# Optimization experiments

Measured on AMD Instinct MI355X. Metric: run time of the kernel, lower is better.

The kernel has to match this reference:

```python
import jax, jax.numpy as jnp
import numpy as np

DIM = 768
H = 12
HD = 64  # head_dim = dim // num_heads
SCALE = HD ** (-0.5)
EPS = 1e-6


def setup_inputs() -> dict:
    key = jax.random.key(0)
    k1, k2, k3, k4, k5 = jax.random.split(key, 5)
    B, N = 8, 1024
    x = jax.random.normal(k1, (B, N, DIM), dtype=jnp.float32)
    policy = jax.random.uniform(k2, (B, N, 1), dtype=jnp.float32)
    # nn.Linear weights: [out_features, in_features]; qkv_bias=False, proj has bias
    qkv_w = jax.random.normal(k3, (3 * H * HD, DIM), dtype=jnp.float32) * (DIM ** -0.5)
    proj_w = jax.random.normal(k4, (DIM, H * HD), dtype=jnp.float32) * ((H * HD) ** -0.5)
    proj_b = jax.random.normal(k5, (DIM,), dtype=jnp.float32) * 0.01
    return {"x": x, "policy": policy, "qkv_w": qkv_w, "proj_w": proj_w, "proj_b": proj_b}


def _softmax_with_policy(attn, policy):
    # attn: [B,H,N,N], policy: [B,N,1]
    B, Hh, N, _ = attn.shape
    attn_policy = policy.reshape(B, 1, 1, N)
    eye = jnp.eye(N, dtype=attn_policy.dtype).reshape(1, 1, N, N)
    attn_policy = attn_policy + (1.0 - attn_policy) * eye
    max_att = jnp.max(attn, axis=-1, keepdims=True)
    a = jnp.exp((attn - max_att).astype(jnp.float32)) * attn_policy.astype(jnp.float32)
    a = (a + EPS / N) / (jnp.sum(a, axis=-1, keepdims=True) + EPS)
    return a.astype(max_att.dtype)


def reference(x, policy, qkv_w, proj_w, proj_b):
    B, N, C = x.shape
    qkv = (x @ qkv_w.T).reshape(B, N, 3, H, HD)
    qkv = jnp.transpose(qkv, (2, 0, 3, 1, 4))  # [3,B,H,N,HD]
    q, k, v = qkv[0], qkv[1], qkv[2]
    attn = jnp.einsum('bhnd,bhmd->bhnm', q * SCALE, k)  # [B,H,N,N]
    attn = _softmax_with_policy(attn, policy)
    out = jnp.einsum('bhnm,bhmd->bhnd', attn, v)  # [B,H,N,HD]
    out = jnp.transpose(out, (0, 2, 1, 3)).reshape(B, N, H * HD)
    return out @ proj_w.T + proj_b
```

## Files before the change

### kernel.cpp

```cpp
#include <hip/hip_runtime.h>

typedef __bf16 bf16x8 __attribute__((ext_vector_type(8)));
typedef float floatx4 __attribute__((ext_vector_type(4)));

#define EPSF 1e-6f

__device__ inline unsigned short f2bf(float f) {
  union { float f; unsigned u; } x; x.f = f;
  unsigned r = x.u + 0x7FFFu + ((x.u >> 16) & 1u);
  return (unsigned short)(r >> 16);
}
__device__ inline float bf2f(unsigned short u) {
  union { unsigned u; float f; } x; x.u = ((unsigned)u) << 16;
  return x.f;
}
__device__ inline unsigned pk2bf(float lo, float hi) {
  union { float f; unsigned u; } a, b; a.f = lo; b.f = hi;
  unsigned ua = a.u + 0x8000u, ub = b.u + 0x8000u;
  return (ub & 0xFFFF0000u) | (ua >> 16);
}
__device__ inline float fexp2(float x) { return __builtin_amdgcn_exp2f(x); }

__device__ inline floatx4 mfma16(bf16x8 a, bf16x8 b, floatx4 c) {
  return __builtin_amdgcn_mfma_f32_16x16x32_bf16(a, b, c, 0, 0, 0);
}

__device__ inline void gll16(const unsigned short* g, unsigned short* l) {
  __builtin_amdgcn_global_load_lds((__attribute__((address_space(1))) void*)g,
                                   (__attribute__((address_space(3))) void*)l, 16, 0, 0);
}

__device__ __host__ inline int sigma_inv(int p) {
  const int qq = p >> 3, jj = p & 7;
  return (jj < 4) ? (qq * 4 + jj) : (16 + qq * 4 + jj - 4);
}

__global__ __launch_bounds__(256) void prep_kernel(const float* __restrict__ x,
                                                   const float* __restrict__ qkv_w,
                                                   const float* __restrict__ proj_w,
                                                   const float* __restrict__ policy,
                                                   unsigned short* __restrict__ xb,
                                                   unsigned short* __restrict__ wqkv,
                                                   unsigned short* __restrict__ wproj,
                                                   unsigned short* __restrict__ pbf) {
  const int bid = blockIdx.x, tid = threadIdx.x;
  if (bid < 3072) {
    const int i = bid * 2048 + tid * 8;
    float4 v0 = *(const float4*)(x + i);
    float4 v1 = *(const float4*)(x + i + 4);
    __align__(16) unsigned short o[8] = {f2bf(v0.x), f2bf(v0.y), f2bf(v0.z), f2bf(v0.w),
                                         f2bf(v1.x), f2bf(v1.y), f2bf(v1.z), f2bf(v1.w)};
    *(float4*)(xb + i) = *(float4*)o;
  } else if (bid < 3936) {
    const int i = (bid - 3072) * 2048 + tid * 8;
    const float s = (i < 589824) ? 0.18033688011112042f : 1.0f;
    float4 v0 = *(const float4*)(qkv_w + i);
    float4 v1 = *(const float4*)(qkv_w + i + 4);
    __align__(16) unsigned short o[8] = {
        f2bf(v0.x * s), f2bf(v0.y * s), f2bf(v0.z * s), f2bf(v0.w * s),
        f2bf(v1.x * s), f2bf(v1.y * s), f2bf(v1.z * s), f2bf(v1.w * s)};
    *(float4*)(wqkv + i) = *(float4*)o;
  } else if (bid < 4224) {
    const int i0 = (bid - 3936) * 2048 + tid * 8;
    const int base = (i0 / 768) * 768 + ((i0 % 768) & ~63);
    __align__(16) unsigned short o[8];
#pragma unroll
    for (int t = 0; t < 8; t++) {
      const int cp = (i0 + t) & 63;
      const int c = 16 * (cp & 3) + (cp >> 2);
      o[t] = f2bf(proj_w[base + c]);
    }
    *(float4*)(wproj + i0) = *(float4*)o;
  } else {
    const int idx = (bid - 4224) * 256 + tid;
    const int b = idx >> 10, g = idx & 1023;
    const int c = ((g >> 5) << 5) + sigma_inv(g & 31);
    pbf[idx] = f2bf(policy[b * 1024 + c]);
  }
}

template <int EP, int BN, int W>
__global__ __launch_bounds__(256, W) void gemm_bt(const unsigned short* __restrict__ A,
                                                  const unsigned short* __restrict__ Bt,
                                                  void* __restrict__ Cout,
                                                  const float* __restrict__ bias,
                                                  int M, int N, int K) {
  constexpr int J = BN / 32;
  __shared__ __align__(16) unsigned short sA[128 * 64];
  __shared__ __align__(16) unsigned short sB[BN * 64];
  const int bid = blockIdx.x;
  const int yb = (bid & 7) * 8 + ((bid >> 3) & 7);
  const int xb_ = bid >> 6;
  const int m0 = yb * 128, n0 = xb_ * BN;
  const int tid = threadIdx.x;
  const int lane = tid & 63, wave = tid >> 6;
  const int qd = lane >> 4, l15 = lane & 15;
  const int wr = (wave >> 1) * 64, wc = (wave & 1) * (BN / 2);
  const int srow = tid >> 3;
  const int scb = (tid & 7) ^ (srow & 7);
  const unsigned short* Ag = A + (long)(m0 + srow) * K + scb * 8;
  const unsigned short* Bg = Bt + (long)(n0 + srow) * K + scb * 8;
  const int x7 = l15 & 7;
  floatx4 acc[4][J] = {};
  for (int k0 = 0; k0 < K; k0 += 64) {
    __syncthreads();
#pragma unroll
    for (int p = 0; p < 4; p++) gll16(Ag + (long)(p * 32) * K + k0, sA + p * 2048 + wave * 512);
#pragma unroll
    for (int p = 0; p < J; p++) gll16(Bg + (long)(p * 32) * K + k0, sB + p * 2048 + wave * 512);
    __syncthreads();
#pragma unroll
    for (int s = 0; s < 2; s++) {
      const int cw = ((s * 4 + qd) ^ x7) * 8;
      bf16x8 af[4], bf[J];
#pragma unroll
      for (int i = 0; i < 4; i++) af[i] = *(const bf16x8*)&sA[(wr + i * 16 + l15) * 64 + cw];
#pragma unroll
      for (int j = 0; j < J; j++) bf[j] = *(const bf16x8*)&sB[(wc + j * 16 + l15) * 64 + cw];
#pragma unroll
      for (int i = 0; i < 4; i++)
#pragma unroll
        for (int j = 0; j < J; j++) acc[i][j] = mfma16(af[i], bf[j], acc[i][j]);
    }
  }
  if constexpr (EP == 0) {
#pragma unroll
    for (int i = 0; i < 4; i++)
#pragma unroll
      for (int r = 0; r < 4; r++) {
        const int row = m0 + wr + i * 16 + qd * 4 + r;
        __align__(8) unsigned short pk[4];
#pragma unroll
        for (int j = 0; j < 4; j++) pk[j] = f2bf(acc[i][j][r]);
        *(uint2*)((unsigned short*)Cout + (long)row * N + n0 + wc + 4 * l15) = *(uint2*)pk;
      }
  } else {
#pragma unroll
    for (int i = 0; i < 4; i++)
#pragma unroll
      for (int j = 0; j < J; j++) {
        const int col = n0 + wc + j * 16 + l15;
#pragma unroll
        for (int r = 0; r < 4; r++) {
          const int row = m0 + wr + i * 16 + qd * 4 + r;
          ((float*)Cout)[(long)row * N + col] = acc[i][j][r] + bias[col];
        }
      }
  }
}

__global__ __launch_bounds__(256) void transpose_v(const unsigned short* __restrict__ qkv,
                                                   const float* __restrict__ policy,
                                                   unsigned short* __restrict__ vTp) {
  __shared__ unsigned short tile[64][72];
  __shared__ float sPol[64];
  const int bh = blockIdx.y;
  const int b = bh / 12, h = bh % 12;
  const int n0 = blockIdx.x * 64;
  const int t = threadIdx.x;
  if (t < 64) sPol[t] = policy[b * 1024 + n0 + t];
  {
    const int nr = t >> 2, dc = (t & 3) * 16;
    const unsigned short* src = qkv + (long)(b * 1024 + n0 + nr) * 2304 + 2 * 768 + h * 64 + dc;
    float4 v0 = *(const float4*)src;
    float4 v1 = *(const float4*)(src + 8);
    *(float4*)&tile[nr][dc] = v0;
    *(float4*)&tile[nr][dc + 8] = v1;
  }
  __syncthreads();
  {
    const int d = t >> 2, nc = (t & 3) * 16;
    __align__(16) unsigned short o[16];
#pragma unroll
    for (int jj = 0; jj < 16; jj++) {
      const int cc = nc + jj;
      const int cl = (cc & 32) + sigma_inv(cc & 31);
      o[jj] = f2bf(bf2f(tile[cl][d]) * sPol[cl]);
    }
    unsigned short* dst = vTp + (long)(bh * 64 + d) * 1024 + n0 + nc;
    *(float4*)dst = *(float4*)&o[0];
    *(float4*)(dst + 8) = *(float4*)&o[8];
  }
}

__global__ __launch_bounds__(256, 3) void attn_kernel(const unsigned short* __restrict__ qkv,
                                                      const unsigned short* __restrict__ vTp,
                                                      const unsigned short* __restrict__ pbf,
                                                      const float* __restrict__ policy,
                                                      unsigned short* __restrict__ aout) {
  __shared__ __align__(16) unsigned short sK[2][2048];
  __shared__ __align__(16) unsigned short sV[2][2048];
  __shared__ __align__(16) unsigned short sPv[1024];
  __shared__ float sD[4][32];
  const int bid = blockIdx.x;
  const int bh = bid % 96, qt = bid / 96;
  const int b = bh / 12, h = bh % 12;
  const int tid = threadIdx.x;
  const int wave = tid >> 6, lane = tid & 63;
  const int qd = lane >> 4, l15 = lane & 15;
  const int q0 = qt * 128 + wave * 32;
  const unsigned short* qb = qkv + (long)(b * 1024 + q0 + l15) * 2304 + h * 64 + qd * 8;
  bf16x8 qf00 = *(const bf16x8*)qb;
  bf16x8 qf01 = *(const bf16x8*)(qb + 32);
  bf16x8 qf10 = *(const bf16x8*)(qb + (long)16 * 2304);
  bf16x8 qf11 = *(const bf16x8*)(qb + (long)16 * 2304 + 32);
  if (tid < 128) *(float4*)(sPv + tid * 8) = *(const float4*)(pbf + b * 1024 + tid * 8);
  const int krow = wave * 8 + (lane >> 3);
  const int kcb = (lane & 7) ^ (lane >> 3);
  const unsigned short* kgl = qkv + (long)(b * 1024 + krow) * 2304 + 768 + h * 64 + kcb * 8;
  const int vrow = tid >> 2;
  const int vcb = (tid & 3) ^ ((vrow ^ (vrow >> 2)) & 3);
  const unsigned short* vgl = vTp + (long)(bh * 64 + vrow) * 1024 + vcb * 8;
  const int x7 = l15 & 7;
  const int vsw = (qd ^ ((l15 ^ (l15 >> 2)) & 3)) * 8;
  floatx4 O0[4] = {}, O1[4] = {};
  floatx4 Dl0 = {}, Dl1 = {};
  gll16(kgl, &sK[0][wave * 512]);
  gll16(vgl, &sV[0][wave * 512]);
  __builtin_amdgcn_s_waitcnt(0);
  __syncthreads();
  for (int it = 0; it < 32; ++it) {
    const int buf = it & 1;
    if (it < 31) {
      gll16(kgl + (long)(32 * (it + 1)) * 2304, &sK[buf ^ 1][wave * 512]);
      gll16(vgl + 32 * (it + 1), &sV[buf ^ 1][wave * 512]);
    }
    const int c0 = it * 32;
    bf16x8 k00 = *(const bf16x8*)&sK[buf][(0 * 16 + l15) * 64 + ((0 + qd) ^ x7) * 8];
    bf16x8 k01 = *(const bf16x8*)&sK[buf][(0 * 16 + l15) * 64 + ((4 + qd) ^ x7) * 8];
    bf16x8 k10 = *(const bf16x8*)&sK[buf][(1 * 16 + l15) * 64 + ((0 + qd) ^ x7) * 8];
    bf16x8 k11 = *(const bf16x8*)&sK[buf][(1 * 16 + l15) * 64 + ((4 + qd) ^ x7) * 8];
    bf16x8 pv = *(const bf16x8*)&sPv[c0 + qd * 8];
    floatx4 z = {0.f, 0.f, 0.f, 0.f};
    floatx4 tA0 = mfma16(k01, qf01, mfma16(k00, qf00, z));
    floatx4 tB0 = mfma16(k11, qf01, mfma16(k10, qf00, z));
    floatx4 tA1 = mfma16(k01, qf11, mfma16(k00, qf10, z));
    floatx4 tB1 = mfma16(k11, qf11, mfma16(k10, qf10, z));
    uint4 pu0, pu1;
    pu0.x = pk2bf(fexp2(tA0[0]), fexp2(tA0[1]));
    pu0.y = pk2bf(fexp2(tA0[2]), fexp2(tA0[3]));
    pu0.z = pk2bf(fexp2(tB0[0]), fexp2(tB0[1]));
    pu0.w = pk2bf(fexp2(tB0[2]), fexp2(tB0[3]));
    pu1.x = pk2bf(fexp2(tA1[0]), fexp2(tA1[1]));
    pu1.y = pk2bf(fexp2(tA1[2]), fexp2(tA1[3]));
    pu1.z = pk2bf(fexp2(tB1[0]), fexp2(tB1[1]));
    pu1.w = pk2bf(fexp2(tB1[2]), fexp2(tB1[3]));
    bf16x8 pf0 = *(bf16x8*)&pu0;
    bf16x8 pf1 = *(bf16x8*)&pu1;
    bf16x8 vf0 = *(const bf16x8*)&sV[buf][(0 * 16 + l15) * 32 + vsw];
    bf16x8 vf1 = *(const bf16x8*)&sV[buf][(1 * 16 + l15) * 32 + vsw];
    bf16x8 vf2 = *(const bf16x8*)&sV[buf][(2 * 16 + l15) * 32 + vsw];
    bf16x8 vf3 = *(const bf16x8*)&sV[buf][(3 * 16 + l15) * 32 + vsw];
    Dl0 = mfma16(pf0, pv, Dl0);
    Dl1 = mfma16(pf1, pv, Dl1);
    O0[0] = mfma16(pf0, vf0, O0[0]); O1[0] = mfma16(pf1, vf0, O1[0]);
    O0[1] = mfma16(pf0, vf1, O0[1]); O1[1] = mfma16(pf1, vf1, O1[1]);
    O0[2] = mfma16(pf0, vf2, O0[2]); O1[2] = mfma16(pf1, vf2, O1[2]);
    O0[3] = mfma16(pf0, vf3, O0[3]); O1[3] = mfma16(pf1, vf3, O1[3]);
    __builtin_amdgcn_s_waitcnt(0);
    __syncthreads();
  }
  {
    const unsigned short* kd = qkv + (long)(b * 1024 + q0 + l15) * 2304 + 768 + h * 64 + qd * 8;
    bf16x8 kd00 = *(const bf16x8*)kd;
    bf16x8 kd01 = *(const bf16x8*)(kd + 32);
    bf16x8 kd10 = *(const bf16x8*)(kd + (long)16 * 2304);
    bf16x8 kd11 = *(const bf16x8*)(kd + (long)16 * 2304 + 32);
    float part0 = 0.f, part1 = 0.f;
#pragma unroll
    for (int jj = 0; jj < 8; jj++) {
      part0 += (float)qf00[jj] * (float)kd00[jj] + (float)qf01[jj] * (float)kd01[jj];
      part1 += (float)qf10[jj] * (float)kd10[jj] + (float)qf11[jj] * (float)kd11[jj];
    }
    part0 += __shfl_xor(part0, 16); part0 += __shfl_xor(part0, 32);
    part1 += __shfl_xor(part1, 16); part1 += __shfl_xor(part1, 32);
    const float p0 = policy[b * 1024 + q0 + l15];
    const float p1 = policy[b * 1024 + q0 + 16 + l15];
    if (qd == 0) {
      sD[wave][l15] = fexp2(part0) * (1.0f - p0);
      sD[wave][16 + l15] = fexp2(part1) * (1.0f - p1);
    }
    __builtin_amdgcn_s_waitcnt(0);
    const unsigned short* vdiag = qkv + (long)(b * 1024 + q0) * 2304 + 1536 + h * 64 + l15;
#pragma unroll
    for (int r = 0; r < 4; r++) {
      const int row = qd * 4 + r;
      const float c0v = sD[wave][row], c1v = sD[wave][16 + row];
#pragma unroll
      for (int j = 0; j < 4; j++) {
        O0[j][r] += c0v * bf2f(vdiag[(long)row * 2304 + j * 16]);
        O1[j][r] += c1v * bf2f(vdiag[(long)(16 + row) * 2304 + j * 16]);
      }
      Dl0[r] += c0v;
      Dl1[r] += c1v;
    }
  }
  const long ob = (long)(b * 1024 + q0 + qd * 4) * 768 + h * 64 + l15;
#pragma unroll
  for (int r = 0; r < 4; r++) {
    const float li0 = 1.0f / (Dl0[r] + EPSF);
    const float li1 = 1.0f / (Dl1[r] + EPSF);
#pragma unroll
    for (int j = 0; j < 4; j++) {
      aout[ob + (long)r * 768 + j * 16] = f2bf(O0[j][r] * li0);
      aout[ob + (long)(16 * 768) + r * 768 + j * 16] = f2bf(O1[j][r] * li1);
    }
  }
}

extern "C" void kernel_launch(void* const* d_in, const int* in_sizes, int n_in,
                              void* d_out, int out_size, void* d_ws, size_t ws_size,
                              hipStream_t stream) {
  const float* x      = (const float*)d_in[0];
  const float* policy = (const float*)d_in[1];
  const float* qkv_w  = (const float*)d_in[2];
  const float* proj_w = (const float*)d_in[3];
  const float* proj_b = (const float*)d_in[4];
  float* out = (float*)d_out;

  char* ws = (char*)d_ws;
  unsigned short* xb    = (unsigned short*)(ws + 0);
  unsigned short* wqkv  = (unsigned short*)(ws + 12582912);
  unsigned short* wproj = (unsigned short*)(ws + 16121856);
  unsigned short* qkvb  = (unsigned short*)(ws + 17301504);
  unsigned short* vTp   = (unsigned short*)(ws + 55050240);
  unsigned short* aoutb = (unsigned short*)(ws + 67633152);
  unsigned short* pbf   = (unsigned short*)(ws + 80216064);

  prep_kernel<<<4256, 256, 0, stream>>>(x, qkv_w, proj_w, policy, xb, wqkv, wproj, pbf);
  gemm_bt<0, 128, 4><<<dim3(18 * 64), 256, 0, stream>>>(xb, wqkv, qkvb, nullptr, 8192, 2304, 768);
  transpose_v<<<dim3(16, 96), 256, 0, stream>>>(qkvb, policy, vTp);
  attn_kernel<<<dim3(768), 256, 0, stream>>>(qkvb, vTp, pbf, policy, aoutb);
  gemm_bt<1, 64, 3><<<dim3(12 * 64), 256, 0, stream>>>(aoutb, wproj, out, proj_b, 8192, 768, 768);
}
```

Baseline: 175.6 us.

## Software-pipeline QK^T one tile ahead with triple-buffered V in attention loop

Restructures the attention main loop so the QK^T MFMAs for the next key tile are issued in the same iteration as the exp/PV work of the current tile. Global prefetch runs two tiles ahead, K stays double-buffered and V moves to a triple buffer so the in-flight loads do not overwrite tiles still being read. The aim is to overlap the exp2 VALU work with matrix-core work and hide load latency. In exchange it uses more LDS and more registers, which could reduce occupancy at launch bounds of 3 blocks.

```diff
diff --git a/kernel.cpp b/kernel.cpp
--- a/kernel.cpp
+++ b/kernel.cpp
@@ -189,7 +189,7 @@
                                                       const float* __restrict__ policy,
                                                       unsigned short* __restrict__ aout) {
   __shared__ __align__(16) unsigned short sK[2][2048];
-  __shared__ __align__(16) unsigned short sV[2][2048];
+  __shared__ __align__(16) unsigned short sV[3][2048];
   __shared__ __align__(16) unsigned short sPv[1024];
   __shared__ float sD[4][32];
   const int bid = blockIdx.x;
@@ -215,27 +215,30 @@
   const int vsw = (qd ^ ((l15 ^ (l15 >> 2)) & 3)) * 8;
   floatx4 O0[4] = {}, O1[4] = {};
   floatx4 Dl0 = {}, Dl1 = {};
+  const floatx4 z = {0.f, 0.f, 0.f, 0.f};
   gll16(kgl, &sK[0][wave * 512]);
   gll16(vgl, &sV[0][wave * 512]);
+  gll16(kgl + (long)32 * 2304, &sK[1][wave * 512]);
+  gll16(vgl + 32, &sV[1][wave * 512]);
   __builtin_amdgcn_s_waitcnt(0);
   __syncthreads();
+  floatx4 tA0, tB0, tA1, tB1;
+  {
+    bf16x8 k00 = *(const bf16x8*)&sK[0][(0 * 16 + l15) * 64 + ((0 + qd) ^ x7) * 8];
+    bf16x8 k01 = *(const bf16x8*)&sK[0][(0 * 16 + l15) * 64 + ((4 + qd) ^ x7) * 8];
+    bf16x8 k10 = *(const bf16x8*)&sK[0][(1 * 16 + l15) * 64 + ((0 + qd) ^ x7) * 8];
+    bf16x8 k11 = *(const bf16x8*)&sK[0][(1 * 16 + l15) * 64 + ((4 + qd) ^ x7) * 8];
+    tA0 = mfma16(k01, qf01, mfma16(k00, qf00, z));
+    tB0 = mfma16(k11, qf01, mfma16(k10, qf00, z));
+    tA1 = mfma16(k01, qf11, mfma16(k00, qf10, z));
+    tB1 = mfma16(k11, qf11, mfma16(k10, qf10, z));
+  }
   for (int it = 0; it < 32; ++it) {
-    const int buf = it & 1;
-    if (it < 31) {
-      gll16(kgl + (long)(32 * (it + 1)) * 2304, &sK[buf ^ 1][wave * 512]);
-      gll16(vgl + 32 * (it + 1), &sV[buf ^ 1][wave * 512]);
-    }
-    const int c0 = it * 32;
-    bf16x8 k00 = *(const bf16x8*)&sK[buf][(0 * 16 + l15) * 64 + ((0 + qd) ^ x7) * 8];
-    bf16x8 k01 = *(const bf16x8*)&sK[buf][(0 * 16 + l15) * 64 + ((4 + qd) ^ x7) * 8];
-    bf16x8 k10 = *(const bf16x8*)&sK[buf][(1 * 16 + l15) * 64 + ((0 + qd) ^ x7) * 8];
-    bf16x8 k11 = *(const bf16x8*)&sK[buf][(1 * 16 + l15) * 64 + ((4 + qd) ^ x7) * 8];
-    bf16x8 pv = *(const bf16x8*)&sPv[c0 + qd * 8];
-    floatx4 z = {0.f, 0.f, 0.f, 0.f};
-    floatx4 tA0 = mfma16(k01, qf01, mfma16(k00, qf00, z));
-    floatx4 tB0 = mfma16(k11, qf01, mfma16(k10, qf00, z));
-    floatx4 tA1 = mfma16(k01, qf11, mfma16(k00, qf10, z));
-    floatx4 tB1 = mfma16(k11, qf11, mfma16(k10, qf10, z));
+    if (it + 2 < 32) {
+      const long cn = 32 * (it + 2);
+      gll16(kgl + cn * 2304, &sK[it & 1][wave * 512]);
+      gll16(vgl + cn, &sV[(it + 2) % 3][wave * 512]);
+    }
     uint4 pu0, pu1;
     pu0.x = pk2bf(fexp2(tA0[0]), fexp2(tA0[1]));
     pu0.y = pk2bf(fexp2(tA0[2]), fexp2(tA0[3]));
@@ -247,10 +250,23 @@
     pu1.w = pk2bf(fexp2(tB1[2]), fexp2(tB1[3]));
     bf16x8 pf0 = *(bf16x8*)&pu0;
     bf16x8 pf1 = *(bf16x8*)&pu1;
-    bf16x8 vf0 = *(const bf16x8*)&sV[buf][(0 * 16 + l15) * 32 + vsw];
-    bf16x8 vf1 = *(const bf16x8*)&sV[buf][(1 * 16 + l15) * 32 + vsw];
-    bf16x8 vf2 = *(const bf16x8*)&sV[buf][(2 * 16 + l15) * 32 + vsw];
-    bf16x8 vf3 = *(const bf16x8*)&sV[buf][(3 * 16 + l15) * 32 + vsw];
+    if (it + 1 < 32) {
+      const unsigned short* kb = &sK[(it + 1) & 1][0];
+      bf16x8 k00 = *(const bf16x8*)&kb[(0 * 16 + l15) * 64 + ((0 + qd) ^ x7) * 8];
+      bf16x8 k01 = *(const bf16x8*)&kb[(0 * 16 + l15) * 64 + ((4 + qd) ^ x7) * 8];
+      bf16x8 k10 = *(const bf16x8*)&kb[(1 * 16 + l15) * 64 + ((0 + qd) ^ x7) * 8];
+      bf16x8 k11 = *(const bf16x8*)&kb[(1 * 16 + l15) * 64 + ((4 + qd) ^ x7) * 8];
+      tA0 = mfma16(k01, qf01, mfma16(k00, qf00, z));
+      tB0 = mfma16(k11, qf01, mfma16(k10, qf00, z));
+      tA1 = mfma16(k01, qf11, mfma16(k00, qf10, z));
+      tB1 = mfma16(k11, qf11, mfma16(k10, qf10, z));
+    }
+    const unsigned short* vb = &sV[it % 3][0];
+    bf16x8 pv = *(const bf16x8*)&sPv[it * 32 + qd * 8];
+    bf16x8 vf0 = *(const bf16x8*)&vb[(0 * 16 + l15) * 32 + vsw];
+    bf16x8 vf1 = *(const bf16x8*)&vb[(1 * 16 + l15) * 32 + vsw];
+    bf16x8 vf2 = *(const bf16x8*)&vb[(2 * 16 + l15) * 32 + vsw];
+    bf16x8 vf3 = *(const bf16x8*)&vb[(3 * 16 + l15) * 32 + vsw];
     Dl0 = mfma16(pf0, pv, Dl0);
     Dl1 = mfma16(pf1, pv, Dl1);
     O0[0] = mfma16(pf0, vf0, O0[0]); O1[0] = mfma16(pf1, vf0, O1[0]);
```

Result: slower. 181.4 us (+3.3%).
